# Performance work log

Measured on AMD Instinct MI355X. Metric: run time of the kernel, lower is better.

Reference implementation:

```python
import jax, jax.numpy as jnp
import numpy as np

# norse Izhikevich 'tonic spiking' behavior constants
A, B_P, C_P, D_P = 0.02, 0.2, -65.0, 6.0
TAU_DT = 250.0 * 0.001  # tau_inv * dt
SQ, MN, BIAS, V_TH = 0.04, 5.0, 140.0, 30.0
V0, U0 = -70.0, -14.0  # initial v, u = b*v
ALPHA = 100.0  # super-spike surrogate slope


@jax.custom_vjp
def super_spike(x):
    return (x > 0).astype(x.dtype)


def _ss_fwd(x):
    return super_spike(x), x


def _ss_bwd(x, g):
    return (g / (ALPHA * jnp.abs(x) + 1.0) ** 2,)


super_spike.defvjp(_ss_fwd, _ss_bwd)


def izh_step(i, v, u):
    # norse izhikevich_step
    v_ = v + TAU_DT * (SQ * v * v + MN * v + BIAS - u + i)
    u_ = u + TAU_DT * A * (B_P * v - u)
    z = super_spike(v_ - V_TH)
    v_new = (1.0 - z) * v_ + z * C_P
    u_new = (1.0 - z) * u_ + z * (u_ + D_P)
    return z, v_new, u_new


def setup_inputs() -> dict:
    key = jax.random.key(0)
    T, Bsz, C = 1000, 512, 64
    ks = jax.random.split(key, 8)
    xs = jax.random.normal(ks[0], (T, Bsz, C), dtype=jnp.float32)
    gaining_factor = 1.0
    bnd_c = 1.0 / np.sqrt(C)
    bnd_2 = 1.0 / np.sqrt(2.0)
    # gaining_layer_1: Linear(C, C) with all-ones weight * gaining_factor, default bias
    W1 = jnp.full((C, C), gaining_factor, dtype=jnp.float32)
    b1 = jax.random.uniform(ks[1], (C,), minval=-bnd_c, maxval=bnd_c, dtype=jnp.float32)
    # Linear(C, 2)
    W2 = jax.random.uniform(ks[2], (2, C), minval=-bnd_c, maxval=bnd_c, dtype=jnp.float32)
    b2 = jax.random.uniform(ks[3], (2,), minval=-bnd_c, maxval=bnd_c, dtype=jnp.float32)
    # gaining_layer_2: Linear(2, 2) with all-ones weight * gaining_factor, default bias
    Wg2 = jnp.full((2, 2), gaining_factor, dtype=jnp.float32)
    bg2 = jax.random.uniform(ks[4], (2,), minval=-bnd_2, maxval=bnd_2, dtype=jnp.float32)
    # Linear(2, 1)
    W3 = jax.random.uniform(ks[5], (1, 2), minval=-bnd_2, maxval=bnd_2, dtype=jnp.float32)
    b3 = jax.random.uniform(ks[6], (1,), minval=-bnd_2, maxval=bnd_2, dtype=jnp.float32)
    return {"xs": xs, "W1": W1, "b1": b1, "W2": W2, "b2": b2,
            "Wg2": Wg2, "bg2": bg2, "W3": W3, "b3": b3}


def reference(xs, W1, b1, W2, b2, Wg2, bg2, W3, b3):
    Bsz = xs.shape[1]
    dt = xs.dtype
    v1 = jnp.full((Bsz, 2), V0, dt); u1 = jnp.full((Bsz, 2), U0, dt)
    v2 = jnp.full((Bsz, 1), V0, dt); u2 = jnp.full((Bsz, 1), U0, dt)

    def step(carry, x):
        v1, u1, v2, u2 = carry
        h = x @ W1.T + b1          # gaining layer 1 [B, C]
        h = h @ W2.T + b2          # [B, 2]
        z1, v1, u1 = izh_step(h, v1, u1)
        g = z1 @ Wg2.T + bg2       # gaining layer 2 [B, 2]
        g = g @ W3.T + b3          # [B, 1]
        z2, v2, u2 = izh_step(g, v2, u2)
        return (v1, u1, v2, u2), z2

    _, spikes = jax.lax.scan(step, (v1, u1, v2, u2), xs)
    return spikes  # [T, B, 1]
```

## Files before the change

### kernel.cpp

```cpp
#include <hip/hip_runtime.h>

#define T_STEPS 1000
#define BSZ     512
#define CDIM    64
#define CHUNK   32
#define NCHUNK  32
#define TAILN   8

__global__ __launch_bounds__(256) void rowsum_kernel(const float* __restrict__ xs,
                                                     float* __restrict__ s) {
    int g   = blockIdx.x * 256 + threadIdx.x;
    int row = g >> 4;
    int sub = g & 15;
    float4 v = reinterpret_cast<const float4*>(xs)[row * 16 + sub];
    float t = (v.x + v.y) + (v.z + v.w);
    t += __shfl_xor(t, 1);
    t += __shfl_xor(t, 2);
    t += __shfl_xor(t, 4);
    t += __shfl_xor(t, 8);
    if (sub == 0) s[row] = t;
}


#define PSTEP(SV, KBIT)                                                    \
    {                                                                      \
        const float iq = fmaf((SV), Sq, cq);                               \
        float a  = fmaf(-0.25f, u, iq);                                    \
        float vp = fmaf(0.01f, v * v, fmaf(2.25f, v, a));                  \
        float up = fmaf(0.005f, fmaf(0.2f, v, -u), u);                     \
        bool z = vp > 30.0f;                                               \
        v = z ? -65.0f : vp;                                               \
        u = z ? u + 6.0f : up;                                             \
        dst[(KBIT) * 64] = z ? Gq : 0.0f;                                  \
    }

#define CSTEP(R0, R1, KBIT)                                                \
    {                                                                      \
        const float g2q = ((R0) + (R1)) + c3q;                             \
        float a2  = fmaf(-0.25f, u2, g2q);                                 \
        float vp2 = fmaf(0.01f, v2 * v2, fmaf(2.25f, v2, a2));             \
        float up2 = fmaf(0.005f, fmaf(0.2f, v2, -u2), u2);                 \
        bool z2 = vp2 > 30.0f;                                             \
        v2 = z2 ? -65.0f : vp2;                                            \
        u2 = z2 ? u2 + 6.0f : up2;                                         \
        acc |= z2 ? (1u << (KBIT)) : 0u;                                   \
    }

__global__ __launch_bounds__(192, 1) void recurrence_kernel(
    const float* __restrict__ b1, const float* __restrict__ W2,
    const float* __restrict__ b2, const float* __restrict__ Wg2,
    const float* __restrict__ bg2, const float* __restrict__ W3,
    const float* __restrict__ b3, const float* __restrict__ s,
    unsigned* __restrict__ bits) {
    const int wave = threadIdx.x >> 6;
    const int lane = threadIdx.x & 63;
    const int b = blockIdx.x * 64 + lane;

    __shared__ float gbuf[2][2][CHUNK][64];

    float S20 = 0.f, S21 = 0.f, d0 = 0.f, d1 = 0.f;
#pragma unroll
    for (int j = 0; j < CDIM; ++j) {
        float w0 = W2[j], w1 = W2[CDIM + j], bj = b1[j];
        S20 += w0; S21 += w1;
        d0 += w0 * bj; d1 += w1 * bj;
    }
    const float S20q = 0.25f * S20;
    const float S21q = 0.25f * S21;
    const float c20q = 0.25f * (d0 + b2[0]) + 35.0f;
    const float c21q = 0.25f * (d1 + b2[1]) + 35.0f;
    const float w30 = W3[0], w31 = W3[1];
    const float G0q = 0.25f * (Wg2[0] * w30 + Wg2[2] * w31);
    const float G1q = 0.25f * (Wg2[1] * w30 + Wg2[3] * w31);
    const float c3q = 0.25f * (bg2[0] * w30 + bg2[1] * w31 + b3[0]) + 35.0f;

    if (wave < 2) {
        const float Sq = wave ? S21q : S20q;
        const float cq = wave ? c21q : c20q;
        const float Gq = wave ? G1q : G0q;
        const int stream = wave;

        float v = -70.f, u = -14.f;
        const float* sp = s + b;

#define LOADP(C, R)                                                        \
        {                                                                  \
            const int base = (C) * CHUNK;                                  \
            _Pragma("unroll")                                              \
            for (int k = 0; k < CHUNK; ++k) {                              \
                int t = base + k;                                          \
                t = t > T_STEPS - 1 ? T_STEPS - 1 : t;                     \
                R[k] = sp[t * BSZ];                                        \
            }                                                              \
        }

#define PPHASE(C, R, NSTEP)                                                \
        {                                                                  \
            float* dst = &gbuf[(C) & 1][stream][0][lane];                  \
            _Pragma("unroll")                                              \
            for (int k = 0; k < (NSTEP); ++k) PSTEP(R[k], k)               \
        }

        float R0[CHUNK], R1[CHUNK], R2[CHUNK];
        LOADP(0, R0)
        LOADP(1, R1)

        for (int j = 0; j < 10; ++j) {
            const int c0 = 3 * j;
            LOADP(c0 + 2, R2)
            PPHASE(c0, R0, CHUNK)
            __syncthreads();
            LOADP(c0 + 3, R0)
            PPHASE(c0 + 1, R1, CHUNK)
            __syncthreads();
            LOADP(c0 + 4, R1)
            PPHASE(c0 + 2, R2, CHUNK)
            __syncthreads();
        }
        PPHASE(30, R0, CHUNK)
        __syncthreads();
        PPHASE(31, R1, TAILN)
        __syncthreads();
        __syncthreads();
#undef LOADP
#undef PPHASE
    } else {
        float v2 = -70.f, u2 = -14.f;
        unsigned accPrev = 0;
        __syncthreads();
        for (int p = 1; p <= NCHUNK; ++p) {
            const int c = p - 1;
            if (p > 1) bits[(c - 1) * BSZ + b] = accPrev;
            const float* src = &gbuf[c & 1][0][0][lane];
            unsigned acc = 0;
            if (c < NCHUNK - 1) {
                float r0[CHUNK], r1[CHUNK];
#pragma unroll
                for (int k = 0; k < CHUNK; ++k) r0[k] = src[k * 64];
#pragma unroll
                for (int k = 0; k < CHUNK; ++k) r1[k] = src[CHUNK * 64 + k * 64];
#pragma unroll
                for (int k = 0; k < CHUNK; ++k) CSTEP(r0[k], r1[k], k)
            } else {
                float r0[TAILN], r1[TAILN];
#pragma unroll
                for (int k = 0; k < TAILN; ++k) r0[k] = src[k * 64];
#pragma unroll
                for (int k = 0; k < TAILN; ++k) r1[k] = src[CHUNK * 64 + k * 64];
#pragma unroll
                for (int k = 0; k < TAILN; ++k) CSTEP(r0[k], r1[k], k)
            }
            accPrev = acc;
            __syncthreads();
        }
        bits[(NCHUNK - 1) * BSZ + b] = accPrev;
    }
}

__global__ __launch_bounds__(256) void expand_kernel(const unsigned* __restrict__ bits,
                                                     float* __restrict__ out) {
    int g = blockIdx.x * 256 + threadIdx.x;
    int t = g >> 9;
    int b = g & 511;
    unsigned w = bits[(t >> 5) * BSZ + b];
    out[g] = (float)((w >> (t & 31)) & 1u);
}

extern "C" void kernel_launch(void* const* d_in, const int* in_sizes, int n_in,
                              void* d_out, int out_size, void* d_ws, size_t ws_size,
                              hipStream_t stream) {
    const float* xs  = (const float*)d_in[0];
    const float* b1  = (const float*)d_in[2];
    const float* W2  = (const float*)d_in[3];
    const float* b2  = (const float*)d_in[4];
    const float* Wg2 = (const float*)d_in[5];
    const float* bg2 = (const float*)d_in[6];
    const float* W3  = (const float*)d_in[7];
    const float* b3  = (const float*)d_in[8];
    float* out = (float*)d_out;
    unsigned* bits = (unsigned*)d_ws;

    const int rows = T_STEPS * BSZ;
    const int blocksA = rows * 16 / 256;
    rowsum_kernel<<<blocksA, 256, 0, stream>>>(xs, out);
    recurrence_kernel<<<8, 192, 0, stream>>>(b1, W2, b2, Wg2, bg2, W3, b3, out, bits);
    expand_kernel<<<rows / 256, 256, 0, stream>>>(bits, out);
}
```

Baseline: 69.43 us.

## Interleave producer streams in LDS for float2 reads and shorten neuron dependency chain

The shared buffer is reordered so the two producer waves' per-step values sit next to each other. The consumer wave can then read both with one float2 LDS load instead of two scalar loads. The Izhikevich update is also rewritten as a Horner-form v*(0.01v+2.25)+a and a single-FMA u update, with u+6 computed ahead of the select, to shorten the serial dependency chain per timestep. The producers now do strided-by-2 scalar stores, which may cause LDS bank conflicts, and the reassociated arithmetic can change spike timing slightly through rounding.

```diff
diff --git a/kernel.cpp b/kernel.cpp
--- a/kernel.cpp
+++ b/kernel.cpp
@@ -22,28 +22,32 @@
 }
 
 
-#define PSTEP(SV, KBIT)                                                    \
+#define PSTEP(SV, KK)                                                      \
     {                                                                      \
-        const float iq = fmaf((SV), Sq, cq);                               \
-        float a  = fmaf(-0.25f, u, iq);                                    \
-        float vp = fmaf(0.01f, v * v, fmaf(2.25f, v, a));                  \
-        float up = fmaf(0.005f, fmaf(0.2f, v, -u), u);                     \
+        const float iq   = fmaf((SV), Sq, cq);                             \
+        const float a    = fmaf(-0.25f, u, iq);                            \
+        const float poly = fmaf(0.01f, v, 2.25f);                          \
+        const float vp   = fmaf(v, poly, a);                               \
+        const float up   = fmaf(0.995f, u, 0.001f * v);                    \
+        const float nu   = u + 6.0f;                                       \
         bool z = vp > 30.0f;                                               \
         v = z ? -65.0f : vp;                                               \
-        u = z ? u + 6.0f : up;                                             \
-        dst[(KBIT) * 64] = z ? Gq : 0.0f;                                  \
+        u = z ? nu : up;                                                   \
+        dst[(KK) * 128] = z ? Gq : 0.0f;                                   \
     }
 
-#define CSTEP(R0, R1, KBIT)                                                \
+#define CSTEP(R01, KK)                                                     \
     {                                                                      \
-        const float g2q = ((R0) + (R1)) + c3q;                             \
-        float a2  = fmaf(-0.25f, u2, g2q);                                 \
-        float vp2 = fmaf(0.01f, v2 * v2, fmaf(2.25f, v2, a2));             \
-        float up2 = fmaf(0.005f, fmaf(0.2f, v2, -u2), u2);                 \
+        const float g2q  = ((R01).x + (R01).y) + c3q;                      \
+        const float a2   = fmaf(-0.25f, u2, g2q);                          \
+        const float poly2 = fmaf(0.01f, v2, 2.25f);                        \
+        const float vp2  = fmaf(v2, poly2, a2);                            \
+        const float up2  = fmaf(0.995f, u2, 0.001f * v2);                  \
+        const float nu2  = u2 + 6.0f;                                      \
         bool z2 = vp2 > 30.0f;                                             \
         v2 = z2 ? -65.0f : vp2;                                            \
-        u2 = z2 ? u2 + 6.0f : up2;                                         \
-        acc |= z2 ? (1u << (KBIT)) : 0u;                                   \
+        u2 = z2 ? nu2 : up2;                                               \
+        acc |= z2 ? (1u << (KK)) : 0u;                                     \
     }
 
 __global__ __launch_bounds__(192, 1) void recurrence_kernel(
@@ -52,11 +56,12 @@
     const float* __restrict__ bg2, const float* __restrict__ W3,
     const float* __restrict__ b3, const float* __restrict__ s,
     unsigned* __restrict__ bits) {
+
+    __shared__ float gbuf[2][CHUNK][64][2];
+
     const int wave = threadIdx.x >> 6;
     const int lane = threadIdx.x & 63;
     const int b = blockIdx.x * 64 + lane;
-
-    __shared__ float gbuf[2][2][CHUNK][64];
 
     float S20 = 0.f, S21 = 0.f, d0 = 0.f, d1 = 0.f;
 #pragma unroll
@@ -96,7 +101,7 @@
 
 #define PPHASE(C, R, NSTEP)                                                \
         {                                                                  \
-            float* dst = &gbuf[(C) & 1][stream][0][lane];                  \
+            float* dst = &gbuf[(C) & 1][0][lane][stream];                  \
             _Pragma("unroll")                                              \
             for (int k = 0; k < (NSTEP); ++k) PSTEP(R[k], k)               \
         }
@@ -131,24 +136,20 @@
         for (int p = 1; p <= NCHUNK; ++p) {
             const int c = p - 1;
             if (p > 1) bits[(c - 1) * BSZ + b] = accPrev;
-            const float* src = &gbuf[c & 1][0][0][lane];
+            const float2* src = reinterpret_cast<const float2*>(&gbuf[c & 1][0][lane][0]);
             unsigned acc = 0;
             if (c < NCHUNK - 1) {
-                float r0[CHUNK], r1[CHUNK];
+                float2 r[CHUNK];
 #pragma unroll
-                for (int k = 0; k < CHUNK; ++k) r0[k] = src[k * 64];
+                for (int k = 0; k < CHUNK; ++k) r[k] = src[k * 64];
 #pragma unroll
-                for (int k = 0; k < CHUNK; ++k) r1[k] = src[CHUNK * 64 + k * 64];
+                for (int k = 0; k < CHUNK; ++k) CSTEP(r[k], k)
+            } else {
+                float2 r[TAILN];
 #pragma unroll
-                for (int k = 0; k < CHUNK; ++k) CSTEP(r0[k], r1[k], k)
-            } else {
-                float r0[TAILN], r1[TAILN];
+                for (int k = 0; k < TAILN; ++k) r[k] = src[k * 64];
 #pragma unroll
-                for (int k = 0; k < TAILN; ++k) r0[k] = src[k * 64];
-#pragma unroll
-                for (int k = 0; k < TAILN; ++k) r1[k] = src[CHUNK * 64 + k * 64];
-#pragma unroll
-                for (int k = 0; k < TAILN; ++k) CSTEP(r0[k], r1[k], k)
+                for (int k = 0; k < TAILN; ++k) CSTEP(r[k], k)
             }
             accPrev = acc;
             __syncthreads();
```

Result: slower. 72.06 us (+3.8%).
